# Kernel tuning notes

Hardware: AMD Instinct MI355X
Metric: run time of the kernel (lower is better)

Reference implementation:

```python
import jax, jax.numpy as jnp
import numpy as np
from jax import lax

ITERATIONS = 10
B, I, D, J, E = 512, 7, 512, 64, 128


def setup_inputs() -> dict:
    key = jax.random.key(0)
    k1, k2, k3 = jax.random.split(key, 3)
    f_bid = jax.random.normal(k1, (B, I, D), dtype=jnp.float32)
    p_bi = jax.random.uniform(k2, (B, I), dtype=jnp.float32)
    weights = jax.random.normal(k3, (I, D, J, E), dtype=jnp.float32)
    return {"f_bid": f_bid, "p_bi": p_bi, "weights": weights}


def reference(f_bid, p_bi, weights):
    # Precompute the per-capsule vote tensor once: [B, I, J, E]
    f_W_bije = jnp.einsum('bid,idje->bije', f_bid, weights)
    b = f_bid.shape[0]
    j, e = weights.shape[2], weights.shape[3]
    c0 = jnp.ones((b, j, e), dtype=f_bid.dtype)

    def body(c_bj, _):
        # routing logits over output capsules j, softmax over j (dim=-1 of 'bij')
        r_bij = jax.nn.softmax(jnp.einsum('bije,bje->bij', f_W_bije, c_bj), axis=-1)
        c_next = jnp.einsum('bi,bij,bije->bje', p_bi, r_bij, f_W_bije)
        return c_next, r_bij

    c_bj, r_stack = lax.scan(body, c0, None, length=ITERATIONS)
    return c_bj, r_stack[-1]
```

## Files before the change

### kernel.cpp

```cpp
#include <hip/hip_runtime.h>
#include <hip/hip_bf16.h>

#define B_SZ 512
#define I_SZ 7
#define D_SZ 512
#define J_SZ 64
#define E_SZ 128
#define N_SZ 8192
#define ITERS 10

typedef __attribute__((ext_vector_type(8))) short bf16x8;
typedef __attribute__((ext_vector_type(4))) float f32x4;

#define AST 40
#define BST 40

#if defined(__has_builtin)
#if __has_builtin(__builtin_amdgcn_cvt_pk_bf16_f32)
#define HAVE_CVT_PK_BF16 1
#endif
#endif

__device__ inline void split2(float x0, float x1, unsigned& hp, unsigned& lp) {
#ifdef HAVE_CVT_PK_BF16
    auto h = __builtin_amdgcn_cvt_pk_bf16_f32(x0, x1);
    hp = __builtin_bit_cast(unsigned, h);
    union { unsigned u; float f; } b0, b1;
    b0.u = hp << 16;
    b1.u = hp & 0xFFFF0000u;
    auto l = __builtin_amdgcn_cvt_pk_bf16_f32(x0 - b0.f, x1 - b1.f);
    lp = __builtin_bit_cast(unsigned, l);
#else
    union { float f; unsigned u; } u0, u1;
    u0.f = x0; u1.f = x1;
    unsigned r0 = u0.u + 0x7FFF + ((u0.u >> 16) & 1);
    unsigned r1 = u1.u + 0x7FFF + ((u1.u >> 16) & 1);
    hp = __builtin_amdgcn_perm(r1, r0, 0x07060302);
    union { unsigned u; float f; } h0, h1;
    h0.u = r0 & 0xFFFF0000u;
    h1.u = r1 & 0xFFFF0000u;
    union { float f; unsigned u; } s0, s1;
    s0.f = x0 - h0.f; s1.f = x1 - h1.f;
    unsigned q0 = s0.u + 0x7FFF + ((s0.u >> 16) & 1);
    unsigned q1 = s1.u + 0x7FFF + ((s1.u >> 16) & 1);
    lp = __builtin_amdgcn_perm(q1, q0, 0x07060302);
#endif
}

__global__ __launch_bounds__(256) void vote_gemm_mfma(
    const float* __restrict__ f,
    const float* __restrict__ W,
    float* __restrict__ fW)
{
    const int i  = blockIdx.z;
    const int m0 = blockIdx.y * 128;
    const int n0 = blockIdx.x * 128;
    const int th = threadIdx.x;

    __shared__ short As_hi[128 * AST], As_lo[128 * AST];
    __shared__ short Bs_hi[128 * BST], Bs_lo[128 * BST];

    const int am  = th >> 1;
    const int akg = th & 1;
    const int bn  = th & 127;
    const int bkh = th >> 7;

    const float* fA = f + (size_t)(m0 + am) * (I_SZ * D_SZ) + (size_t)i * D_SZ + akg * 16;
    const float* WB = W + (size_t)i * D_SZ * N_SZ + n0 + bn;

    const int wave = th >> 6, lane = th & 63;
    const int wr = wave >> 1, wc = wave & 1;
    const int lm = lane & 15, quad = lane >> 4;

    f32x4 acc[4][4];
#pragma unroll
    for (int a = 0; a < 4; ++a)
#pragma unroll
        for (int c = 0; c < 4; ++c)
            acc[a][c] = (f32x4){0.f, 0.f, 0.f, 0.f};

    float av[16], bv[16];
    {
        float4 t0 = *(const float4*)(fA);
        float4 t1 = *(const float4*)(fA + 4);
        float4 t2 = *(const float4*)(fA + 8);
        float4 t3 = *(const float4*)(fA + 12);
        av[0]=t0.x; av[1]=t0.y; av[2]=t0.z; av[3]=t0.w;
        av[4]=t1.x; av[5]=t1.y; av[6]=t1.z; av[7]=t1.w;
        av[8]=t2.x; av[9]=t2.y; av[10]=t2.z; av[11]=t2.w;
        av[12]=t3.x; av[13]=t3.y; av[14]=t3.z; av[15]=t3.w;
        const float* pb = WB + (size_t)(bkh * 16) * N_SZ;
#pragma unroll
        for (int r = 0; r < 16; ++r) bv[r] = pb[(size_t)r * N_SZ];
    }

    for (int k0 = 0; k0 < D_SZ; k0 += 32) {
        uint4 ah0, al0, ah1, al1, bh0, bl0, bh1, bl1;
        split2(av[0],  av[1],  ah0.x, al0.x);
        split2(av[2],  av[3],  ah0.y, al0.y);
        split2(av[4],  av[5],  ah0.z, al0.z);
        split2(av[6],  av[7],  ah0.w, al0.w);
        split2(av[8],  av[9],  ah1.x, al1.x);
        split2(av[10], av[11], ah1.y, al1.y);
        split2(av[12], av[13], ah1.z, al1.z);
        split2(av[14], av[15], ah1.w, al1.w);
        split2(bv[0],  bv[1],  bh0.x, bl0.x);
        split2(bv[2],  bv[3],  bh0.y, bl0.y);
        split2(bv[4],  bv[5],  bh0.z, bl0.z);
        split2(bv[6],  bv[7],  bh0.w, bl0.w);
        split2(bv[8],  bv[9],  bh1.x, bl1.x);
        split2(bv[10], bv[11], bh1.y, bl1.y);
        split2(bv[12], bv[13], bh1.z, bl1.z);
        split2(bv[14], bv[15], bh1.w, bl1.w);

        __syncthreads();
        *(uint4*)&As_hi[am * AST + akg * 16]     = ah0;
        *(uint4*)&As_hi[am * AST + akg * 16 + 8] = ah1;
        *(uint4*)&As_lo[am * AST + akg * 16]     = al0;
        *(uint4*)&As_lo[am * AST + akg * 16 + 8] = al1;
        *(uint4*)&Bs_hi[bn * BST + bkh * 16]     = bh0;
        *(uint4*)&Bs_hi[bn * BST + bkh * 16 + 8] = bh1;
        *(uint4*)&Bs_lo[bn * BST + bkh * 16]     = bl0;
        *(uint4*)&Bs_lo[bn * BST + bkh * 16 + 8] = bl1;
        __syncthreads();

        if (k0 + 32 < D_SZ) {
            const float* pa = fA + k0 + 32;
            float4 t0 = *(const float4*)(pa);
            float4 t1 = *(const float4*)(pa + 4);
            float4 t2 = *(const float4*)(pa + 8);
            float4 t3 = *(const float4*)(pa + 12);
            av[0]=t0.x; av[1]=t0.y; av[2]=t0.z; av[3]=t0.w;
            av[4]=t1.x; av[5]=t1.y; av[6]=t1.z; av[7]=t1.w;
            av[8]=t2.x; av[9]=t2.y; av[10]=t2.z; av[11]=t2.w;
            av[12]=t3.x; av[13]=t3.y; av[14]=t3.z; av[15]=t3.w;
            const float* pb = WB + (size_t)(k0 + 32 + bkh * 16) * N_SZ;
#pragma unroll
            for (int r = 0; r < 16; ++r) bv[r] = pb[(size_t)r * N_SZ];
        }

        bf16x8 Ah[4], Al[4], Bh[4], Bl[4];
#pragma unroll
        for (int t = 0; t < 4; ++t) {
            const int ar = (wr * 64 + t * 16 + lm) * AST + quad * 8;
            Ah[t] = *(const bf16x8*)&As_hi[ar];
            Al[t] = *(const bf16x8*)&As_lo[ar];
            const int br = (wc * 64 + t * 16 + lm) * BST + quad * 8;
            Bh[t] = *(const bf16x8*)&Bs_hi[br];
            Bl[t] = *(const bf16x8*)&Bs_lo[br];
        }
#pragma unroll
        for (int tm = 0; tm < 4; ++tm)
#pragma unroll
            for (int tn = 0; tn < 4; ++tn) {
                acc[tm][tn] = __builtin_amdgcn_mfma_f32_16x16x32_bf16(Ah[tm], Bh[tn], acc[tm][tn], 0, 0, 0);
                acc[tm][tn] = __builtin_amdgcn_mfma_f32_16x16x32_bf16(Ah[tm], Bl[tn], acc[tm][tn], 0, 0, 0);
                acc[tm][tn] = __builtin_amdgcn_mfma_f32_16x16x32_bf16(Al[tm], Bh[tn], acc[tm][tn], 0, 0, 0);
            }
    }

#pragma unroll
    for (int tm = 0; tm < 4; ++tm) {
        const int rowb = m0 + wr * 64 + tm * 16 + quad * 4;
#pragma unroll
        for (int tn = 0; tn < 4; ++tn) {
            const int col = n0 + wc * 64 + tn * 16 + lm;
#pragma unroll
            for (int r = 0; r < 4; ++r)
                fW[((size_t)(rowb + r) * I_SZ + i) * N_SZ + col] = acc[tm][tn][r];
        }
    }
}

__global__ __launch_bounds__(1024) void routing_kernel(
    const float* __restrict__ fW,
    const float* __restrict__ p,
    float* __restrict__ c_out,
    float* __restrict__ r_out)
{
    const int b   = blockIdx.x;
    const int tid = threadIdx.x;
    const int j   = tid >> 4;
    const int sub = tid & 15;

    __shared__ float G_sh[64][49];
    __shared__ float s_sh[64][9];
    __shared__ float w_sh[2][64][9];
    __shared__ float p_sh[8];

    if (tid < I_SZ) p_sh[tid] = p[(size_t)b * I_SZ + tid];

    float4 fw[I_SZ][2];
    const float* base = fW + (size_t)b * I_SZ * N_SZ + j * E_SZ + sub * 8;
#pragma unroll
    for (int i = 0; i < I_SZ; ++i) {
        fw[i][0] = *(const float4*)(base + (size_t)i * N_SZ);
        fw[i][1] = *(const float4*)(base + (size_t)i * N_SZ + 4);
    }

#pragma unroll
    for (int i = 0; i < I_SZ; ++i) {
        float s = fw[i][0].x + fw[i][0].y + fw[i][0].z + fw[i][0].w
                + fw[i][1].x + fw[i][1].y + fw[i][1].z + fw[i][1].w;
        s += __shfl_xor(s, 1); s += __shfl_xor(s, 2);
        s += __shfl_xor(s, 4); s += __shfl_xor(s, 8);
        if (sub == 0) s_sh[j][i] = s;
#pragma unroll
        for (int i2 = i; i2 < I_SZ; ++i2) {
            float g = fw[i][0].x * fw[i2][0].x + fw[i][0].y * fw[i2][0].y
                    + fw[i][0].z * fw[i2][0].z + fw[i][0].w * fw[i2][0].w
                    + fw[i][1].x * fw[i2][1].x + fw[i][1].y * fw[i2][1].y
                    + fw[i][1].z * fw[i2][1].z + fw[i][1].w * fw[i2][1].w;
            g += __shfl_xor(g, 1); g += __shfl_xor(g, 2);
            g += __shfl_xor(g, 4); g += __shfl_xor(g, 8);
            if (sub == 0) { G_sh[j][i * 7 + i2] = g; G_sh[j][i2 * 7 + i] = g; }
        }
    }
    __syncthreads();

    for (int t = 0; t < ITERS; ++t) {
        if (tid < I_SZ * 64) {
            const int ii = tid >> 6;
            const int jj = tid & 63;
            float l;
            if (t == 0) {
                l = s_sh[jj][ii];
            } else {
                const int rb = t & 1;
                l = 0.f;
#pragma unroll
                for (int i2 = 0; i2 < I_SZ; ++i2)
                    l = fmaf(w_sh[rb][jj][i2], G_sh[jj][ii * 7 + i2], l);
            }
            float mx = l;
#pragma unroll
            for (int off = 32; off > 0; off >>= 1)
                mx = fmaxf(mx, __shfl_xor(mx, off));
            float ex = __expf(l - mx);
            float sm = ex;
#pragma unroll
            for (int off = 32; off > 0; off >>= 1)
                sm += __shfl_xor(sm, off);
            float r = ex / sm;
            if (t == ITERS - 1)
                r_out[(size_t)b * (I_SZ * J_SZ) + ii * 64 + jj] = r;
            w_sh[(t + 1) & 1][jj][ii] = p_sh[ii] * r;
        }
        __syncthreads();
    }

    float4 a0 = make_float4(0.f, 0.f, 0.f, 0.f);
    float4 a1 = make_float4(0.f, 0.f, 0.f, 0.f);
#pragma unroll
    for (int i = 0; i < I_SZ; ++i) {
        float wv = w_sh[ITERS & 1][j][i];
        a0.x = fmaf(wv, fw[i][0].x, a0.x); a0.y = fmaf(wv, fw[i][0].y, a0.y);
        a0.z = fmaf(wv, fw[i][0].z, a0.z); a0.w = fmaf(wv, fw[i][0].w, a0.w);
        a1.x = fmaf(wv, fw[i][1].x, a1.x); a1.y = fmaf(wv, fw[i][1].y, a1.y);
        a1.z = fmaf(wv, fw[i][1].z, a1.z); a1.w = fmaf(wv, fw[i][1].w, a1.w);
    }
    float* dst = c_out + (size_t)b * N_SZ + j * E_SZ + sub * 8;
    *(float4*)(dst)     = a0;
    *(float4*)(dst + 4) = a1;
}

extern "C" void kernel_launch(void* const* d_in, const int* in_sizes, int n_in,
                              void* d_out, int out_size, void* d_ws, size_t ws_size,
                              hipStream_t stream) {
    const float* f = (const float*)d_in[0];
    const float* p = (const float*)d_in[1];
    const float* W = (const float*)d_in[2];
    float* out = (float*)d_out;
    float* fW  = (float*)d_ws;

    vote_gemm_mfma<<<dim3(N_SZ / 128, B_SZ / 128, I_SZ), 256, 0, stream>>>(f, W, fW);
    routing_kernel<<<B_SZ, 1024, 0, stream>>>(fW, p, out, out + (size_t)B_SZ * N_SZ);
}
```

Before: 288.5 us.

## Widen vote GEMM tile to 128x256 and drop register prefetch

The vote GEMM block tile grows from 128x128 to 128x256. Each wave now computes a 64x128 sub-tile with 32 accumulators, and each thread loads a full 32-deep column of W. This halves the grid and the number of A-tile reloads, raising MFMA work per shared-memory load. The software prefetch of the next k-slice into registers is removed, so global loads are no longer overlapped with MFMA. Register pressure rises sharply, which risks lower occupancy or spills.

```diff
diff --git a/kernel.cpp b/kernel.cpp
--- a/kernel.cpp
+++ b/kernel.cpp
@@ -12,8 +12,7 @@
 typedef __attribute__((ext_vector_type(8))) short bf16x8;
 typedef __attribute__((ext_vector_type(4))) float f32x4;
 
-#define AST 40
-#define BST 40
+#define LST 40
 
 #if defined(__has_builtin)
 #if __has_builtin(__builtin_amdgcn_cvt_pk_bf16_f32)
@@ -54,78 +53,34 @@
 {
     const int i  = blockIdx.z;
     const int m0 = blockIdx.y * 128;
-    const int n0 = blockIdx.x * 128;
+    const int n0 = blockIdx.x * 256;
     const int th = threadIdx.x;
 
-    __shared__ short As_hi[128 * AST], As_lo[128 * AST];
-    __shared__ short Bs_hi[128 * BST], Bs_lo[128 * BST];
+    __shared__ short As_hi[128 * LST], As_lo[128 * LST];
+    __shared__ short Bs_hi[256 * LST], Bs_lo[256 * LST];
 
     const int am  = th >> 1;
     const int akg = th & 1;
-    const int bn  = th & 127;
-    const int bkh = th >> 7;
+    const int bn  = th;
 
     const float* fA = f + (size_t)(m0 + am) * (I_SZ * D_SZ) + (size_t)i * D_SZ + akg * 16;
     const float* WB = W + (size_t)i * D_SZ * N_SZ + n0 + bn;
 
     const int wave = th >> 6, lane = th & 63;
-    const int wr = wave >> 1, wc = wave & 1;
+    const int wr = wave & 1, wc = wave >> 1;
     const int lm = lane & 15, quad = lane >> 4;
 
-    f32x4 acc[4][4];
+    f32x4 acc[4][8];
 #pragma unroll
     for (int a = 0; a < 4; ++a)
 #pragma unroll
-        for (int c = 0; c < 4; ++c)
+        for (int c = 0; c < 8; ++c)
             acc[a][c] = (f32x4){0.f, 0.f, 0.f, 0.f};
 
-    float av[16], bv[16];
-    {
-        float4 t0 = *(const float4*)(fA);
-        float4 t1 = *(const float4*)(fA + 4);
-        float4 t2 = *(const float4*)(fA + 8);
-        float4 t3 = *(const float4*)(fA + 12);
-        av[0]=t0.x; av[1]=t0.y; av[2]=t0.z; av[3]=t0.w;
-        av[4]=t1.x; av[5]=t1.y; av[6]=t1.z; av[7]=t1.w;
-        av[8]=t2.x; av[9]=t2.y; av[10]=t2.z; av[11]=t2.w;
-        av[12]=t3.x; av[13]=t3.y; av[14]=t3.z; av[15]=t3.w;
-        const float* pb = WB + (size_t)(bkh * 16) * N_SZ;
-#pragma unroll
-        for (int r = 0; r < 16; ++r) bv[r] = pb[(size_t)r * N_SZ];
-    }
-
     for (int k0 = 0; k0 < D_SZ; k0 += 32) {
-        uint4 ah0, al0, ah1, al1, bh0, bl0, bh1, bl1;
-        split2(av[0],  av[1],  ah0.x, al0.x);
-        split2(av[2],  av[3],  ah0.y, al0.y);
-        split2(av[4],  av[5],  ah0.z, al0.z);
-        split2(av[6],  av[7],  ah0.w, al0.w);
-        split2(av[8],  av[9],  ah1.x, al1.x);
-        split2(av[10], av[11], ah1.y, al1.y);
-        split2(av[12], av[13], ah1.z, al1.z);
-        split2(av[14], av[15], ah1.w, al1.w);
-        split2(bv[0],  bv[1],  bh0.x, bl0.x);
-        split2(bv[2],  bv[3],  bh0.y, bl0.y);
-        split2(bv[4],  bv[5],  bh0.z, bl0.z);
-        split2(bv[6],  bv[7],  bh0.w, bl0.w);
-        split2(bv[8],  bv[9],  bh1.x, bl1.x);
-        split2(bv[10], bv[11], bh1.y, bl1.y);
-        split2(bv[12], bv[13], bh1.z, bl1.z);
-        split2(bv[14], bv[15], bh1.w, bl1.w);
-
-        __syncthreads();
-        *(uint4*)&As_hi[am * AST + akg * 16]     = ah0;
-        *(uint4*)&As_hi[am * AST + akg * 16 + 8] = ah1;
-        *(uint4*)&As_lo[am * AST + akg * 16]     = al0;
-        *(uint4*)&As_lo[am * AST + akg * 16 + 8] = al1;
-        *(uint4*)&Bs_hi[bn * BST + bkh * 16]     = bh0;
-        *(uint4*)&Bs_hi[bn * BST + bkh * 16 + 8] = bh1;
-        *(uint4*)&Bs_lo[bn * BST + bkh * 16]     = bl0;
-        *(uint4*)&Bs_lo[bn * BST + bkh * 16 + 8] = bl1;
-        __syncthreads();
-
-        if (k0 + 32 < D_SZ) {
-            const float* pa = fA + k0 + 32;
+        float av[16];
+        {
+            const float* pa = fA + k0;
             float4 t0 = *(const float4*)(pa);
             float4 t1 = *(const float4*)(pa + 4);
             float4 t2 = *(const float4*)(pa + 8);
@@ -134,25 +89,53 @@
             av[4]=t1.x; av[5]=t1.y; av[6]=t1.z; av[7]=t1.w;
             av[8]=t2.x; av[9]=t2.y; av[10]=t2.z; av[11]=t2.w;
             av[12]=t3.x; av[13]=t3.y; av[14]=t3.z; av[15]=t3.w;
-            const float* pb = WB + (size_t)(k0 + 32 + bkh * 16) * N_SZ;
-#pragma unroll
-            for (int r = 0; r < 16; ++r) bv[r] = pb[(size_t)r * N_SZ];
-        }
-
-        bf16x8 Ah[4], Al[4], Bh[4], Bl[4];
+        }
+        float bv[32];
+        {
+            const float* pb = WB + (size_t)k0 * N_SZ;
+#pragma unroll
+            for (int r = 0; r < 32; ++r) bv[r] = pb[(size_t)r * N_SZ];
+        }
+
+        unsigned ahw[8], alw[8];
+#pragma unroll
+        for (int r = 0; r < 8; ++r) split2(av[2 * r], av[2 * r + 1], ahw[r], alw[r]);
+        unsigned bhw[16], blw[16];
+#pragma unroll
+        for (int r = 0; r < 16; ++r) split2(bv[2 * r], bv[2 * r + 1], bhw[r], blw[r]);
+
+        __syncthreads();
+        *(uint4*)&As_hi[am * LST + akg * 16]     = make_uint4(ahw[0], ahw[1], ahw[2], ahw[3]);
+        *(uint4*)&As_hi[am * LST + akg * 16 + 8] = make_uint4(ahw[4], ahw[5], ahw[6], ahw[7]);
+        *(uint4*)&As_lo[am * LST + akg * 16]     = make_uint4(alw[0], alw[1], alw[2], alw[3]);
+        *(uint4*)&As_lo[am * LST + akg * 16 + 8] = make_uint4(alw[4], alw[5], alw[6], alw[7]);
+#pragma unroll
+        for (int s = 0; s < 4; ++s) {
+            *(uint4*)&Bs_hi[bn * LST + s * 8] =
+                make_uint4(bhw[4 * s], bhw[4 * s + 1], bhw[4 * s + 2], bhw[4 * s + 3]);
+            *(uint4*)&Bs_lo[bn * LST + s * 8] =
+                make_uint4(blw[4 * s], blw[4 * s + 1], blw[4 * s + 2], blw[4 * s + 3]);
+        }
+        __syncthreads();
+
+        bf16x8 Ah[4], Al[4];
 #pragma unroll
         for (int t = 0; t < 4; ++t) {
-            const int ar = (wr * 64 + t * 16 + lm) * AST + quad * 8;
+            const int ar = (wr * 64 + t * 16 + lm) * LST + quad * 8;
             Ah[t] = *(const bf16x8*)&As_hi[ar];
             Al[t] = *(const bf16x8*)&As_lo[ar];
-            const int br = (wc * 64 + t * 16 + lm) * BST + quad * 8;
-            Bh[t] = *(const bf16x8*)&Bs_hi[br];
-            Bl[t] = *(const bf16x8*)&Bs_lo[br];
+        }
+        bf16x8 Bh[8], Bl[8];
+#pragma unroll
+        for (int u = 0; u < 8; ++u) {
+            const int br = (wc * 128 + u * 16 + lm) * LST + quad * 8;
+            Bh[u] = *(const bf16x8*)&Bs_hi[br];
+            Bl[u] = *(const bf16x8*)&Bs_lo[br];
         }
 #pragma unroll
         for (int tm = 0; tm < 4; ++tm)
 #pragma unroll
-            for (int tn = 0; tn < 4; ++tn) {
+            for (int tn = 0; tn < 8; ++tn) {
                 acc[tm][tn] = __builtin_amdgcn_mfma_f32_16x16x32_bf16(Ah[tm], Bh[tn], acc[tm][tn], 0, 0, 0);
                 acc[tm][tn] = __builtin_amdgcn_mfma_f32_16x16x32_bf16(Ah[tm], Bl[tn], acc[tm][tn], 0, 0, 0);
                 acc[tm][tn] = __builtin_amdgcn_mfma_f32_16x16x32_bf16(Al[tm], Bh[tn], acc[tm][tn], 0, 0, 0);
@@ -163,8 +146,8 @@
     for (int tm = 0; tm < 4; ++tm) {
         const int rowb = m0 + wr * 64 + tm * 16 + quad * 4;
 #pragma unroll
-        for (int tn = 0; tn < 4; ++tn) {
-            const int col = n0 + wc * 64 + tn * 16 + lm;
+        for (int tn = 0; tn < 8; ++tn) {
+            const int col = n0 + wc * 128 + tn * 16 + lm;
 #pragma unroll
             for (int r = 0; r < 4; ++r)
                 fW[((size_t)(rowb + r) * I_SZ + i) * N_SZ + col] = acc[tm][tn][r];
@@ -273,6 +256,6 @@
     float* out = (float*)d_out;
     float* fW  = (float*)d_ws;
 
-    vote_gemm_mfma<<<dim3(N_SZ / 128, B_SZ / 128, I_SZ), 256, 0, stream>>>(f, W, fW);
+    vote_gemm_mfma<<<dim3(N_SZ / 256, B_SZ / 128, I_SZ), 256, 0, stream>>>(f, W, fW);
     routing_kernel<<<B_SZ, 1024, 0, stream>>>(fW, p, out, out + (size_t)B_SZ * N_SZ);
 }
```

Result: slower. 403.5 us (+39.8%).
